# Kernel tuning notes

Measured on AMD Instinct MI355X. Metric: run time of the kernel, lower is better.

Reference implementation:

```python
import jax, jax.numpy as jnp
import numpy as np

NPOINT = 1024
RADIUS = 0.9
NSAMPLE = 32
MLP = [64, 64, 128]
IN_CH = 67
BN_EPS = 1e-5


def setup_inputs() -> dict:
    key = jax.random.key(0)
    ks = jax.random.split(key, 2 + 2 * len(MLP))
    B, N, C = 16, 4096, 64
    inp = {}
    inp["xyz"] = jax.random.uniform(ks[0], (B, N, 3), dtype=jnp.float32)
    inp["points"] = jax.random.normal(ks[1], (B, N, C), dtype=jnp.float32)
    last = IN_CH
    for i, oc in enumerate(MLP):
        inp[f"w{i}"] = jax.random.normal(ks[2 + 2 * i], (oc, last), dtype=jnp.float32) * (1.0 / np.sqrt(last))
        inp[f"b{i}"] = jax.random.normal(ks[3 + 2 * i], (oc,), dtype=jnp.float32) * 0.01
        inp[f"g{i}"] = jnp.ones((oc,), jnp.float32)
        inp[f"beta{i}"] = jnp.zeros((oc,), jnp.float32)
        last = oc
    return inp


def _farthest_point_sample(xyz, npoint):
    # Sequential FPS; initial farthest index fixed to 0 (torch used randint) for determinism.
    B, N, _ = xyz.shape

    def step(carry, _):
        distance, far = carry
        cen = jnp.take_along_axis(xyz, far[:, None, None], axis=1)  # [B,1,3]
        d = jnp.sum((xyz - cen) ** 2, -1)                            # [B,N]
        distance = jnp.minimum(distance, d)
        new_far = jnp.argmax(distance, axis=-1).astype(jnp.int32)
        return (distance, new_far), far

    init = (jnp.full((B, N), 1e10, xyz.dtype), jnp.zeros((B,), jnp.int32))
    _, cents = jax.lax.scan(step, init, None, length=npoint)  # [npoint, B]
    return jnp.transpose(cents)  # [B, npoint]


def _gather(points, idx):
    # points [B,N,C], idx [B,S] or [B,S,K]
    return jax.vmap(lambda p, i: p[i])(points, idx)


def _query_ball_point(radius, nsample, xyz, new_xyz):
    # Faithful to source: Euclidean distance (cdist p=2) compared against radius**2.
    B, N, _ = xyz.shape
    d2 = (jnp.sum(new_xyz ** 2, -1)[:, :, None]
          + jnp.sum(xyz ** 2, -1)[:, None, :]
          - 2.0 * jnp.einsum('bsc,bnc->bsn', new_xyz, xyz))
    dist = jnp.sqrt(jnp.maximum(d2, 0.0))                  # [B,S,N]
    arang = jnp.arange(N, dtype=jnp.int32)[None, None, :]
    gi = jnp.where(dist > radius ** 2, N, arang)           # [B,S,N]
    gi = jnp.sort(gi, axis=-1)[:, :, :nsample]             # [B,S,K]
    first = gi[:, :, :1]
    gi = jnp.where(gi == N, first, gi)
    return gi


def _forward(xyz, points, params):
    idx = _farthest_point_sample(xyz, NPOINT)              # [B,S]
    new_xyz = _gather(xyz, idx)                            # [B,S,3]
    gidx = _query_ball_point(RADIUS, NSAMPLE, xyz, new_xyz)
    grouped_xyz = _gather(xyz, gidx)                       # [B,S,K,3]
    grouped_xyz_norm = grouped_xyz - new_xyz[:, :, None, :]
    grouped_pts = _gather(points, gidx)                    # [B,S,K,C]
    x = jnp.concatenate([grouped_xyz_norm, grouped_pts], axis=-1)  # [B,S,K,3+C]
    x = jnp.transpose(x, (0, 3, 1, 2))                     # [B,Cin,S,K]
    for (w, b, g, be) in params:
        x = jnp.einsum('oc,bcsk->bosk', w, x) + b[None, :, None, None]
        mu = jnp.mean(x, axis=(0, 2, 3), keepdims=True)    # BN in training mode (batch stats, biased var)
        var = jnp.mean((x - mu) ** 2, axis=(0, 2, 3), keepdims=True)
        x = (x - mu) / jnp.sqrt(var + BN_EPS) * g[None, :, None, None] + be[None, :, None, None]
        x = jax.nn.relu(x)
    new_points = jnp.max(x, axis=-1)                       # [B,Cout,S]
    new_points = jnp.transpose(new_points, (0, 2, 1))      # [B,S,Cout]
    return new_xyz, new_points


def reference(xyz, points, w0, b0, g0, beta0, w1, b1, g1, beta1, w2, b2, g2, beta2):
    params = [(w0, b0, g0, beta0), (w1, b1, g1, beta1), (w2, b2, g2, beta2)]
    return _forward(xyz, points, params)
```

## Files before the change

### kernel.cpp

```cpp
#include <hip/hip_runtime.h>
#include <hip/hip_bf16.h>
#include <stdint.h>

#define BB 16
#define NN 4096
#define NPOINT 1024
#define NSAMPLE 32

typedef unsigned int u32;
typedef unsigned long long u64;
typedef unsigned short u16;
typedef float f32x2 __attribute__((ext_vector_type(2)));
using frag_ab = __attribute__((ext_vector_type(8))) short;
using frag_cd = __attribute__((ext_vector_type(4))) float;

__device__ inline u16 f2bf(float x){ u32 u = __float_as_uint(x); u32 r = (u + 0x7fffu + ((u>>16)&1u)) >> 16; return (u16)r; }
__device__ inline float bf2f(u32 hbits){ return __uint_as_float(hbits<<16); }
__device__ inline u64 umax64(u64 a, u64 b){ return a > b ? a : b; }

__device__ inline int wave_max_bits(float v){
    int x = __float_as_int(v);
    int t;
    t = __builtin_amdgcn_update_dpp(0, x, 0x111, 0xf, 0xf, true);
    x = __float_as_int(fmaxf(__int_as_float(x), __int_as_float(t)));
    t = __builtin_amdgcn_update_dpp(0, x, 0x112, 0xf, 0xf, true);
    x = __float_as_int(fmaxf(__int_as_float(x), __int_as_float(t)));
    t = __builtin_amdgcn_update_dpp(0, x, 0x114, 0xf, 0xf, true);
    x = __float_as_int(fmaxf(__int_as_float(x), __int_as_float(t)));
    t = __builtin_amdgcn_update_dpp(0, x, 0x118, 0xf, 0xf, true);
    x = __float_as_int(fmaxf(__int_as_float(x), __int_as_float(t)));
    t = __builtin_amdgcn_update_dpp(0, x, 0x142, 0xf, 0xf, true);
    x = __float_as_int(fmaxf(__int_as_float(x), __int_as_float(t)));
    t = __builtin_amdgcn_update_dpp(0, x, 0x143, 0xf, 0xf, true);
    x = __float_as_int(fmaxf(__int_as_float(x), __int_as_float(t)));
    return __builtin_amdgcn_readlane(x, 63);
}

__global__ __launch_bounds__(256) void fps_kernel(const float* __restrict__ xyz, int* __restrict__ cents)
{
#pragma clang fp contract(off)
    __shared__ float lxyz[NN*3];
    __shared__ __align__(16) u64 s_red[2][4];
    const int tid = threadIdx.x;
    const int b = blockIdx.x;
    const float* gx = xyz + (size_t)b*NN*3;
    for (int i = tid; i < NN*3; i += 256) lxyz[i] = gx[i];
    __syncthreads();
    f32x2 px[8], py[8], pz[8], dist[8];
#pragma unroll
    for (int jj = 0; jj < 8; jj++){
        int p = tid*16 + jj*2;
        px[jj] = (f32x2){ lxyz[p*3+0], lxyz[(p+1)*3+0] };
        py[jj] = (f32x2){ lxyz[p*3+1], lxyz[(p+1)*3+1] };
        pz[jj] = (f32x2){ lxyz[p*3+2], lxyz[(p+1)*3+2] };
        dist[jj] = (f32x2){ 1e10f, 1e10f };
    }
    const int lane = tid & 63;
    const int wid = tid >> 6;
    int far = 0, par = 0;
    for (int s = 0; s < NPOINT; s++){
        if (tid == 0) cents[b*NPOINT + s] = far;
        float cx = lxyz[far*3+0], cy = lxyz[far*3+1], cz = lxyz[far*3+2];
        f32x2 c2x = { cx, cx }, c2y = { cy, cy }, c2z = { cz, cz };
        f32x2 bm0 = { -1.f, -1.f }, bm1 = { -1.f, -1.f };
#pragma unroll
        for (int jj = 0; jj < 8; jj++){
            f32x2 dx = px[jj] - c2x;
            f32x2 dy = py[jj] - c2y;
            f32x2 dz = pz[jj] - c2z;
            f32x2 d  = (dx*dx + dy*dy) + dz*dz;
            f32x2 nd = __builtin_elementwise_min(dist[jj], d);
            dist[jj] = nd;
            if (jj < 4) bm0 = __builtin_elementwise_max(bm0, nd);
            else        bm1 = __builtin_elementwise_max(bm1, nd);
        }
        f32x2 bmA = __builtin_elementwise_max(bm0, bm1);
        float bv = fmaxf(bmA.x, bmA.y);
        int wmb = wave_max_bits(bv);
        float wmax = __int_as_float(wmb);
        u64 mask = __ballot(bv == wmax);
        int fl = __ffsll((long long)mask) - 1;
        float g0m = fmaxf(bm0.x, bm0.y);
        int gsel = (g0m == wmax) ? 0 : 1;
        u32 mbits = 0;
#pragma unroll
        for (int u = 0; u < 4; u++){
            f32x2 dd = gsel ? dist[4+u] : dist[u];
            if (dd.x == wmax) mbits |= (1u << (2*u));
            if (dd.y == wmax) mbits |= (1u << (2*u+1));
        }
        int fj = (gsel << 3) + (__ffs(mbits) - 1);
        int fjw = __builtin_amdgcn_readlane(fj, fl);
        int p = (wid << 10) + (fl << 4) + fjw;
        if (lane == 0) s_red[par][wid] = ((u64)(u32)wmb << 32) | (u32)(4095 - p);
        __syncthreads();
        uint4 k01 = *(const uint4*)&s_red[par][0];
        uint4 k23 = *(const uint4*)&s_red[par][2];
        u64 r0 = ((u64)k01.y << 32) | k01.x;
        u64 r1 = ((u64)k01.w << 32) | k01.z;
        u64 r2 = ((u64)k23.y << 32) | k23.x;
        u64 r3 = ((u64)k23.w << 32) | k23.z;
        u64 m  = umax64(umax64(r0, r1), umax64(r2, r3));
        far = 4095 - (int)(m & 0xFFFu);
        par ^= 1;
    }
}

__global__ __launch_bounds__(256) void gather_newxyz_kernel(const float* __restrict__ xyz, const int* __restrict__ cents,
                                                            float* __restrict__ out, float* __restrict__ nxyz)
{
    int i = blockIdx.x*256 + threadIdx.x;
    int b = i / 3072;
    int r = i - b*3072;
    int s = r / 3;
    int c = r - s*3;
    int idx = cents[b*NPOINT + s];
    float v = xyz[((size_t)b*NN + idx)*3 + c];
    out[i] = v;
    nxyz[i] = v;
}

__global__ __launch_bounds__(256) void pack_points_kernel(const float* __restrict__ points, u32* __restrict__ pbf)
{
    int i = blockIdx.x*256 + threadIdx.x;
    float f0 = points[2*i], f1 = points[2*i+1];
    pbf[i] = (u32)f2bf(f0) | ((u32)f2bf(f1) << 16);
}

__global__ __launch_bounds__(256) void ballquery_kernel(const float* __restrict__ xyz, const float* __restrict__ nxyz,
                                                        const int* __restrict__ cents, int* __restrict__ gidx)
{
    const int lane = threadIdx.x & 63;
    const int w = (blockIdx.x << 2) + (threadIdx.x >> 6);
    const int b = w >> 10;
    const float RAD2 = (float)(0.9*0.9);
    const float* c3 = nxyz + (size_t)w*3;
    float cx = c3[0], cy = c3[1], cz = c3[2];
    float sc = __fadd_rn(__fadd_rn(__fmul_rn(cx,cx), __fmul_rn(cy,cy)), __fmul_rn(cz,cz));
    const float* gx = xyz + (size_t)b*NN*3;
    int* gout = gidx + (size_t)w*NSAMPLE;
    int found = 0; int first = -1;
    for (int base = 0; base < NN; base += 64){
        int i = base + lane;
        float pxv = gx[i*3+0], pyv = gx[i*3+1], pzv = gx[i*3+2];
        float sp = __fadd_rn(__fadd_rn(__fmul_rn(pxv,pxv), __fmul_rn(pyv,pyv)), __fmul_rn(pzv,pzv));
        float dot = __fadd_rn(__fadd_rn(__fmul_rn(cx,pxv), __fmul_rn(cy,pyv)), __fmul_rn(cz,pzv));
        float d2 = __fsub_rn(__fadd_rn(sc, sp), __fmul_rn(2.0f, dot));
        float dd = __fsqrt_rn(fmaxf(d2, 0.0f));
        bool in = !(dd > RAD2);
        u64 m = __ballot(in);
        int cnt = __popcll(m);
        if (in){
            int slot = found + __popcll(m & ((1ull<<lane) - 1ull));
            if (slot < NSAMPLE) gout[slot] = i;
        }
        if (found == 0 && cnt > 0) first = base + (__ffsll(m) - 1);
        found += cnt;
        if (found >= NSAMPLE) break;
    }
    if (found < NSAMPLE){
        if (found == 0) first = cents[w];
        for (int slot = found + lane; slot < NSAMPLE; slot += 64) gout[slot] = first;
    }
}

__global__ __launch_bounds__(256) void conv1_kernel(const float* __restrict__ xyz, const u32* __restrict__ pbf,
                                                    const float* __restrict__ nxyz, const int* __restrict__ gidx,
                                                    const float* __restrict__ w, const float* __restrict__ bias,
                                                    u32* __restrict__ xout, float* __restrict__ stats)
{
    __shared__ float sxyz[512][3];
    const int tid = threadIdx.x;
    const int lane = tid & 63;
    const int wid = tid >> 6;
    const int quad = lane >> 4;
    const int col = lane & 15;
    const int blockbase = blockIdx.x*512;
    for (int r = tid; r < 512; r += 256){
        int m = blockbase + r;
        int b = m >> 15, s = (m >> 5) & 1023, g = gidx[m];
        const float* p3 = xyz + ((size_t)(b<<12) + g)*3;
        const float* c3 = nxyz + ((size_t)b*NPOINT + s)*3;
        sxyz[r][0] = p3[0]-c3[0]; sxyz[r][1] = p3[1]-c3[1]; sxyz[r][2] = p3[2]-c3[2];
    }
    frag_ab Bf[4][2];
#pragma unroll
    for (int nt = 0; nt < 4; nt++)
#pragma unroll
        for (int kh = 0; kh < 2; kh++){
            const float* wr = w + (nt*16 + col)*67 + 3 + kh*32 + quad*8;
#pragma unroll
            for (int j = 0; j < 8; j++) Bf[nt][kh][j] = (short)f2bf(wr[j]);
        }
    float wx[4], wy[4], wz[4], biasl[4];
#pragma unroll
    for (int nt = 0; nt < 4; nt++){
        const float* wb = w + (nt*16 + col)*67;
        wx[nt] = wb[0]; wy[nt] = wb[1]; wz[nt] = wb[2];
        biasl[nt] = bias[nt*16 + col];
    }
    __syncthreads();
    float ssum[4] = {0,0,0,0}, ssq[4] = {0,0,0,0};
    u16* xo = (u16*)xout;
    const int tile0 = blockIdx.x*32 + wid*8;
#pragma unroll 2
    for (int t = 0; t < 8; t++){
        const int tile = tile0 + t;
        const size_t m0 = (size_t)tile * 16;
        const int b = (int)(m0 >> 15);
        const int g = gidx[m0 + col];
        const u32* arow = pbf + ((size_t)(b<<12) + g)*32;
        uint4 u0 = *(const uint4*)(arow + quad*4);
        uint4 u1 = *(const uint4*)(arow + 16 + quad*4);
        frag_ab Af0, Af1;
        __builtin_memcpy(&Af0, &u0, 16);
        __builtin_memcpy(&Af1, &u1, 16);
        frag_cd acc[4];
#pragma unroll
        for (int nt = 0; nt < 4; nt++){
            acc[nt] = (frag_cd){0.f, 0.f, 0.f, 0.f};
            acc[nt] = __builtin_amdgcn_mfma_f32_16x16x32_bf16(Af0, Bf[nt][0], acc[nt], 0, 0, 0);
            acc[nt] = __builtin_amdgcn_mfma_f32_16x16x32_bf16(Af1, Bf[nt][1], acc[nt], 0, 0, 0);
        }
        const int rbase = (int)(m0 - blockbase) + quad*4;
#pragma unroll
        for (int r = 0; r < 4; r++){
            float xnx = sxyz[rbase+r][0], xny = sxyz[rbase+r][1], xnz = sxyz[rbase+r][2];
#pragma unroll
            for (int nt = 0; nt < 4; nt++){
                float v = acc[nt][r] + biasl[nt];
                v = fmaf(wx[nt], xnx, v);
                v = fmaf(wy[nt], xny, v);
                v = fmaf(wz[nt], xnz, v);
                xo[(m0 + quad*4 + r)*64 + nt*16 + col] = f2bf(v);
                ssum[nt] += v;
                ssq[nt] = fmaf(v, v, ssq[nt]);
            }
        }
    }
#pragma unroll
    for (int nt = 0; nt < 4; nt++){
        ssum[nt] += __shfl_xor(ssum[nt], 16); ssq[nt] += __shfl_xor(ssq[nt], 16);
        ssum[nt] += __shfl_xor(ssum[nt], 32); ssq[nt] += __shfl_xor(ssq[nt], 32);
    }
    if (quad == 0){
        float* st = stats + (blockIdx.x & 7)*256;
#pragma unroll
        for (int nt = 0; nt < 4; nt++){
            atomicAdd(&st[nt*16 + col], ssum[nt]);
            atomicAdd(&st[128 + nt*16 + col], ssq[nt]);
        }
    }
}

__device__ inline void block_finalize(const float* __restrict__ stats, const float* __restrict__ g,
                                      const float* __restrict__ beta, float* saff, int C, int tid)
{
    if (tid < C){
        float sm = 0.f, sq = 0.f;
#pragma unroll
        for (int r = 0; r < 8; r++){ sm += stats[r*256+tid]; sq += stats[r*256+128+tid]; }
        const float invM = 1.0f / 524288.0f;
        float mu  = sm * invM;
        float var = fmaxf(sq * invM - mu*mu, 0.0f);
        float inv = 1.0f / sqrtf(var + 1e-5f);
        float a = g[tid] * inv;
        saff[tid] = a;
        saff[128+tid] = beta[tid] - mu*a;
    }
}

__device__ inline void unpack_affine_relu(uint4 u, const float* ak, const float* bk, short* dst){
    const u32* uu = (const u32*)&u;
#pragma unroll
    for (int q = 0; q < 4; q++){
        u32 v = uu[q];
        float x0 = bf2f(v & 0xffffu);
        float x1 = bf2f(v >> 16);
        float f0 = fmaxf(fmaf(ak[2*q],   x0, bk[2*q]),   0.f);
        float f1 = fmaxf(fmaf(ak[2*q+1], x1, bk[2*q+1]), 0.f);
        dst[2*q]   = (short)f2bf(f0);
        dst[2*q+1] = (short)f2bf(f1);
    }
}

__global__ __launch_bounds__(256) void conv2_kernel(const u32* __restrict__ xin, const float* __restrict__ stats_in,
                                                    const float* __restrict__ gw, const float* __restrict__ beta,
                                                    const float* __restrict__ w, const float* __restrict__ bias,
                                                    u32* __restrict__ xout, float* __restrict__ stats)
{
    __shared__ float saff[256];
    const int tid = threadIdx.x;
    block_finalize(stats_in, gw, beta, saff, 64, tid);
    const int lane = tid & 63;
    const int wid = tid >> 6;
    const int quad = lane >> 4;
    const int col = lane & 15;
    frag_ab Bf[4][2];
#pragma unroll
    for (int nt = 0; nt < 4; nt++)
#pragma unroll
        for (int kh = 0; kh < 2; kh++){
            const float* wr = w + (nt*16 + col)*64 + kh*32 + quad*8;
#pragma unroll
            for (int j = 0; j < 8; j++) Bf[nt][kh][j] = (short)f2bf(wr[j]);
        }
    float biasl[4];
#pragma unroll
    for (int nt = 0; nt < 4; nt++) biasl[nt] = bias[nt*16 + col];
    __syncthreads();
    float ak[2][8], bk[2][8];
#pragma unroll
    for (int kh = 0; kh < 2; kh++)
#pragma unroll
        for (int j = 0; j < 8; j++){
            int k = kh*32 + quad*8 + j;
            ak[kh][j] = saff[k]; bk[kh][j] = saff[128+k];
        }
    float ssum[4] = {0,0,0,0}, ssq[4] = {0,0,0,0};
    u16* xo = (u16*)xout;
    const int tile0 = blockIdx.x*64 + wid*16;
    for (int t = 0; t < 16; t++){
        const size_t m0 = (size_t)(tile0 + t) * 16;
        const u32* arow = xin + (m0 + col)*32;
        uint4 u0 = *(const uint4*)(arow + quad*4);
        uint4 u1 = *(const uint4*)(arow + 16 + quad*4);
        frag_ab Af0, Af1;
        unpack_affine_relu(u0, ak[0], bk[0], (short*)&Af0);
        unpack_affine_relu(u1, ak[1], bk[1], (short*)&Af1);
        frag_cd acc[4];
#pragma unroll
        for (int nt = 0; nt < 4; nt++){
            acc[nt] = (frag_cd){biasl[nt], biasl[nt], biasl[nt], biasl[nt]};
            acc[nt] = __builtin_amdgcn_mfma_f32_16x16x32_bf16(Af0, Bf[nt][0], acc[nt], 0, 0, 0);
            acc[nt] = __builtin_amdgcn_mfma_f32_16x16x32_bf16(Af1, Bf[nt][1], acc[nt], 0, 0, 0);
        }
#pragma unroll
        for (int nt = 0; nt < 4; nt++){
#pragma unroll
            for (int r = 0; r < 4; r++){
                float v = acc[nt][r];
                xo[(m0 + quad*4 + r)*64 + nt*16 + col] = f2bf(v);
                ssum[nt] += v;
                ssq[nt] = fmaf(v, v, ssq[nt]);
            }
        }
    }
#pragma unroll
    for (int nt = 0; nt < 4; nt++){
        ssum[nt] += __shfl_xor(ssum[nt], 16); ssq[nt] += __shfl_xor(ssq[nt], 16);
        ssum[nt] += __shfl_xor(ssum[nt], 32); ssq[nt] += __shfl_xor(ssq[nt], 32);
    }
    if (quad == 0){
        float* st = stats + (blockIdx.x & 7)*256;
#pragma unroll
        for (int nt = 0; nt < 4; nt++){
            atomicAdd(&st[nt*16 + col], ssum[nt]);
            atomicAdd(&st[128 + nt*16 + col], ssq[nt]);
        }
    }
}

__global__ __launch_bounds__(256) void conv3_kernel(const u32* __restrict__ xin, const float* __restrict__ stats_in,
                                                    const float* __restrict__ gw, const float* __restrict__ beta,
                                                    const float* __restrict__ w, const float* __restrict__ bias,
                                                    float* __restrict__ gmax, float* __restrict__ gmin,
                                                    float* __restrict__ stats)
{
    __shared__ float saff[256];
    const int tid = threadIdx.x;
    block_finalize(stats_in, gw, beta, saff, 64, tid);
    const int lane = tid & 63;
    const int wid = tid >> 6;
    const int quad = lane >> 4;
    const int col = lane & 15;
    frag_ab Bf[8][2];
#pragma unroll
    for (int nt = 0; nt < 8; nt++)
#pragma unroll
        for (int kh = 0; kh < 2; kh++){
            const float* wr = w + (nt*16 + col)*64 + kh*32 + quad*8;
#pragma unroll
            for (int j = 0; j < 8; j++) Bf[nt][kh][j] = (short)f2bf(wr[j]);
        }
    float biasl[8];
#pragma unroll
    for (int nt = 0; nt < 8; nt++) biasl[nt] = bias[nt*16 + col];
    __syncthreads();
    float ak[2][8], bk[2][8];
#pragma unroll
    for (int kh = 0; kh < 2; kh++)
#pragma unroll
        for (int j = 0; j < 8; j++){
            int k = kh*32 + quad*8 + j;
            ak[kh][j] = saff[k]; bk[kh][j] = saff[128+k];
        }
    float ssum[8], ssq[8], mx[8], mn[8];
#pragma unroll
    for (int nt = 0; nt < 8; nt++){ ssum[nt] = 0.f; ssq[nt] = 0.f; }
    const int tile0 = blockIdx.x*32 + wid*8;
#pragma unroll 2
    for (int t = 0; t < 8; t++){
        const size_t m0 = (size_t)(tile0 + t) * 16;
        const u32* arow = xin + (m0 + col)*32;
        uint4 u0 = *(const uint4*)(arow + quad*4);
        uint4 u1 = *(const uint4*)(arow + 16 + quad*4);
        frag_ab Af0, Af1;
        unpack_affine_relu(u0, ak[0], bk[0], (short*)&Af0);
        unpack_affine_relu(u1, ak[1], bk[1], (short*)&Af1);
        frag_cd acc[8];
#pragma unroll
        for (int nt = 0; nt < 8; nt++){
            acc[nt] = (frag_cd){biasl[nt], biasl[nt], biasl[nt], biasl[nt]};
            acc[nt] = __builtin_amdgcn_mfma_f32_16x16x32_bf16(Af0, Bf[nt][0], acc[nt], 0, 0, 0);
            acc[nt] = __builtin_amdgcn_mfma_f32_16x16x32_bf16(Af1, Bf[nt][1], acc[nt], 0, 0, 0);
        }
#pragma unroll
        for (int nt = 0; nt < 8; nt++){
            float a0 = fmaxf(fmaxf(acc[nt][0], acc[nt][1]), fmaxf(acc[nt][2], acc[nt][3]));
            float n0 = fminf(fminf(acc[nt][0], acc[nt][1]), fminf(acc[nt][2], acc[nt][3]));
            if ((t & 1) == 0){ mx[nt] = a0; mn[nt] = n0; }
            else { mx[nt] = fmaxf(mx[nt], a0); mn[nt] = fminf(mn[nt], n0); }
#pragma unroll
            for (int r = 0; r < 4; r++){
                float v = acc[nt][r];
                ssum[nt] += v;
                ssq[nt] = fmaf(v, v, ssq[nt]);
            }
        }
        if (t & 1){
#pragma unroll
            for (int nt = 0; nt < 8; nt++){
                mx[nt] = fmaxf(mx[nt], __shfl_xor(mx[nt], 16));
                mn[nt] = fminf(mn[nt], __shfl_xor(mn[nt], 16));
                mx[nt] = fmaxf(mx[nt], __shfl_xor(mx[nt], 32));
                mn[nt] = fminf(mn[nt], __shfl_xor(mn[nt], 32));
            }
            if (quad == 0){
                const int g = (tile0 + t - 1) >> 1;
#pragma unroll
                for (int nt = 0; nt < 8; nt++){
                    gmax[(size_t)g*128 + nt*16 + col] = mx[nt];
                    gmin[(size_t)g*128 + nt*16 + col] = mn[nt];
                }
            }
        }
    }
#pragma unroll
    for (int nt = 0; nt < 8; nt++){
        ssum[nt] += __shfl_xor(ssum[nt], 16); ssq[nt] += __shfl_xor(ssq[nt], 16);
        ssum[nt] += __shfl_xor(ssum[nt], 32); ssq[nt] += __shfl_xor(ssq[nt], 32);
    }
    if (quad == 0){
        float* st = stats + (blockIdx.x & 7)*256;
#pragma unroll
        for (int nt = 0; nt < 8; nt++){
            atomicAdd(&st[nt*16 + col], ssum[nt]);
            atomicAdd(&st[128 + nt*16 + col], ssq[nt]);
        }
    }
}

__global__ __launch_bounds__(256) void pool_kernel(const float* __restrict__ gmax, const float* __restrict__ gmin,
                                                   const float* __restrict__ stats_in, const float* __restrict__ gw,
                                                   const float* __restrict__ beta, float* __restrict__ out)
{
    __shared__ float saff[256];
    const int tid = threadIdx.x;
    block_finalize(stats_in, gw, beta, saff, 128, tid);
    __syncthreads();
    const int base = blockIdx.x*2048 + tid;
#pragma unroll
    for (int k = 0; k < 8; k++){
        int idx = base + k*256;
        int o = idx & 127;
        float a = saff[o], bsh = saff[128+o];
        float v = (a >= 0.f) ? fmaf(a, gmax[idx], bsh) : fmaf(a, gmin[idx], bsh);
        out[(size_t)BB*NPOINT*3 + idx] = fmaxf(v, 0.f);
    }
}

extern "C" void kernel_launch(void* const* d_in, const int* in_sizes, int n_in,
                              void* d_out, int out_size, void* d_ws, size_t ws_size,
                              hipStream_t stream)
{
    const float* xyz    = (const float*)d_in[0];
    const float* points = (const float*)d_in[1];
    const float* w0  = (const float*)d_in[2];
    const float* b0  = (const float*)d_in[3];
    const float* g0  = (const float*)d_in[4];
    const float* be0 = (const float*)d_in[5];
    const float* w1  = (const float*)d_in[6];
    const float* b1  = (const float*)d_in[7];
    const float* g1  = (const float*)d_in[8];
    const float* be1 = (const float*)d_in[9];
    const float* w2  = (const float*)d_in[10];
    const float* b2  = (const float*)d_in[11];
    const float* g2  = (const float*)d_in[12];
    const float* be2 = (const float*)d_in[13];
    float* out = (float*)d_out;
    char* ws = (char*)d_ws;

    int*   cents = (int*)(ws + 0);
    float* nxyz  = (float*)(ws + 65536);
    int*   gidx  = (int*)(ws + 262144);
    float* stats = (float*)(ws + 2359296);
    u32*   x1buf = (u32*)(ws + 2386944);
    u32*   x2buf = (u32*)(ws + 69495808);
    float* gmax  = (float*)(ws + 136604672);
    float* gmin  = (float*)(ws + 144993280);
    u32*   pbf   = (u32*)(ws + 136604672);

    hipMemsetAsync(stats, 0, 6144*sizeof(float), stream);
    fps_kernel<<<16, 256, 0, stream>>>(xyz, cents);
    gather_newxyz_kernel<<<192, 256, 0, stream>>>(xyz, cents, out, nxyz);
    pack_points_kernel<<<8192, 256, 0, stream>>>(points, pbf);
    ballquery_kernel<<<4096, 256, 0, stream>>>(xyz, nxyz, cents, gidx);
    conv1_kernel<<<1024, 256, 0, stream>>>(xyz, pbf, nxyz, gidx, w0, b0, x1buf, stats);
    conv2_kernel<<<512, 256, 0, stream>>>(x1buf, stats, g0, be0, w1, b1, x2buf, stats + 2048);
    conv3_kernel<<<1024, 256, 0, stream>>>(x2buf, stats + 2048, g1, be1, w2, b2, gmax, gmin, stats + 4096);
    pool_kernel<<<1024, 256, 0, stream>>>(gmax, gmin, stats + 4096, g2, be2, out);
}
```

Before: 803.5 us.

## Replace FPS block barrier with tagged LDS spin-wait and forward centroid coordinates

In the farthest-point-sampling loop, the per-iteration __syncthreads is replaced by a flag-based spin-wait. Each wave publishes its max distance, its index and a step tag to LDS, and all threads poll until all four waves have written the current tag. Each wave also publishes the coordinates of its candidate point, so the next centroid comes straight from the reduction instead of a dependent LDS load of lxyz[far]. The per-thread argmax is now tracked inline during the distance update, replacing the separate rescan for matching lanes. The risks are relying on volatile LDS ordering without explicit fences, and a 12-bit tag that wraps, though 1024 steps with double buffering stays within range.

```diff
diff --git a/kernel.cpp b/kernel.cpp
--- a/kernel.cpp
+++ b/kernel.cpp
@@ -16,7 +16,6 @@
 
 __device__ inline u16 f2bf(float x){ u32 u = __float_as_uint(x); u32 r = (u + 0x7fffu + ((u>>16)&1u)) >> 16; return (u16)r; }
 __device__ inline float bf2f(u32 hbits){ return __uint_as_float(hbits<<16); }
-__device__ inline u64 umax64(u64 a, u64 b){ return a > b ? a : b; }
 
 __device__ inline int wave_max_bits(float v){
     int x = __float_as_int(v);
@@ -40,11 +39,13 @@
 {
 #pragma clang fp contract(off)
     __shared__ float lxyz[NN*3];
-    __shared__ __align__(16) u64 s_red[2][4];
+    __shared__ __align__(16) u32 sK[2][8];
+    __shared__ __align__(16) float sC[2][4][4];
     const int tid = threadIdx.x;
     const int b = blockIdx.x;
     const float* gx = xyz + (size_t)b*NN*3;
     for (int i = tid; i < NN*3; i += 256) lxyz[i] = gx[i];
+    if (tid < 8){ sK[0][tid] = 0; sK[1][tid] = 0; }
     __syncthreads();
     f32x2 px[8], py[8], pz[8], dist[8];
 #pragma unroll
@@ -58,50 +59,64 @@
     const int lane = tid & 63;
     const int wid = tid >> 6;
     int far = 0, par = 0;
+    float cx = lxyz[0], cy = lxyz[1], cz = lxyz[2];
     for (int s = 0; s < NPOINT; s++){
         if (tid == 0) cents[b*NPOINT + s] = far;
-        float cx = lxyz[far*3+0], cy = lxyz[far*3+1], cz = lxyz[far*3+2];
         f32x2 c2x = { cx, cx }, c2y = { cy, cy }, c2z = { cz, cz };
-        f32x2 bm0 = { -1.f, -1.f }, bm1 = { -1.f, -1.f };
+        float bv = -1.0f; int bj = 0;
 #pragma unroll
         for (int jj = 0; jj < 8; jj++){
             f32x2 dx = px[jj] - c2x;
             f32x2 dy = py[jj] - c2y;
             f32x2 dz = pz[jj] - c2z;
             f32x2 d  = (dx*dx + dy*dy) + dz*dz;
-            f32x2 nd = __builtin_elementwise_min(dist[jj], d);
+            f32x2 nd;
+            nd.x = fminf(dist[jj].x, d.x);
+            nd.y = fminf(dist[jj].y, d.y);
             dist[jj] = nd;
-            if (jj < 4) bm0 = __builtin_elementwise_max(bm0, nd);
-            else        bm1 = __builtin_elementwise_max(bm1, nd);
-        }
-        f32x2 bmA = __builtin_elementwise_max(bm0, bm1);
-        float bv = fmaxf(bmA.x, bmA.y);
+            if (nd.x > bv){ bv = nd.x; bj = jj*2; }
+            if (nd.y > bv){ bv = nd.y; bj = jj*2+1; }
+        }
+        const int p_loc = tid*16 + bj;
+        float sx = lxyz[p_loc*3+0], sy = lxyz[p_loc*3+1], sz = lxyz[p_loc*3+2];
         int wmb = wave_max_bits(bv);
         float wmax = __int_as_float(wmb);
         u64 mask = __ballot(bv == wmax);
         int fl = __ffsll((long long)mask) - 1;
-        float g0m = fmaxf(bm0.x, bm0.y);
-        int gsel = (g0m == wmax) ? 0 : 1;
-        u32 mbits = 0;
-#pragma unroll
-        for (int u = 0; u < 4; u++){
-            f32x2 dd = gsel ? dist[4+u] : dist[u];
-            if (dd.x == wmax) mbits |= (1u << (2*u));
-            if (dd.y == wmax) mbits |= (1u << (2*u+1));
-        }
-        int fj = (gsel << 3) + (__ffs(mbits) - 1);
-        int fjw = __builtin_amdgcn_readlane(fj, fl);
-        int p = (wid << 10) + (fl << 4) + fjw;
-        if (lane == 0) s_red[par][wid] = ((u64)(u32)wmb << 32) | (u32)(4095 - p);
-        __syncthreads();
-        uint4 k01 = *(const uint4*)&s_red[par][0];
-        uint4 k23 = *(const uint4*)&s_red[par][2];
-        u64 r0 = ((u64)k01.y << 32) | k01.x;
-        u64 r1 = ((u64)k01.w << 32) | k01.z;
-        u64 r2 = ((u64)k23.y << 32) | k23.x;
-        u64 r3 = ((u64)k23.w << 32) | k23.z;
-        u64 m  = umax64(umax64(r0, r1), umax64(r2, r3));
-        far = 4095 - (int)(m & 0xFFFu);
+        int pw = __builtin_amdgcn_readlane(p_loc, fl);
+        float qx = __int_as_float(__builtin_amdgcn_readlane(__float_as_int(sx), fl));
+        float qy = __int_as_float(__builtin_amdgcn_readlane(__float_as_int(sy), fl));
+        float qz = __int_as_float(__builtin_amdgcn_readlane(__float_as_int(sz), fl));
+        const u32 tag = (u32)(s + 1);
+        if (lane == 0){
+            volatile float* vc = &sC[par][wid][0];
+            vc[0] = qx; vc[1] = qy; vc[2] = qz;
+            volatile u32* vk = &sK[par][wid*2];
+            vk[0] = (u32)wmb;
+            vk[1] = ((u32)(4095 - pw) << 12) | tag;
+        }
+        volatile u32* vk = &sK[par][0];
+        u32 t0, t1, t2, t3;
+        for (;;){
+            t0 = vk[1]; t1 = vk[3]; t2 = vk[5]; t3 = vk[7];
+            if ((((t0 ^ tag) | (t1 ^ tag) | (t2 ^ tag) | (t3 ^ tag)) & 0xFFFu) == 0) break;
+        }
+        u32 d0 = vk[0], d1 = vk[2], d2 = vk[4], d3 = vk[6];
+        volatile float* vc = &sC[par][0][0];
+        float x0 = vc[0],  y0 = vc[1],  z0 = vc[2];
+        float x1 = vc[4],  y1 = vc[5],  z1 = vc[6];
+        float x2v= vc[8],  y2 = vc[9],  z2 = vc[10];
+        float x3 = vc[12], y3 = vc[13], z3 = vc[14];
+        u64 k0 = ((u64)d0 << 32) | t0;
+        u64 k1 = ((u64)d1 << 32) | t1;
+        u64 k2 = ((u64)d2 << 32) | t2;
+        u64 k3 = ((u64)d3 << 32) | t3;
+        u64 bk = k0; float bx = x0, by = y0, bz = z0;
+        if (k1 > bk){ bk = k1; bx = x1;  by = y1; bz = z1; }
+        if (k2 > bk){ bk = k2; bx = x2v; by = y2; bz = z2; }
+        if (k3 > bk){ bk = k3; bx = x3;  by = y3; bz = z3; }
+        far = 4095 - (int)(((u32)bk >> 12) & 0xFFFu);
+        cx = bx; cy = by; cz = bz;
         par ^= 1;
     }
 }
```

Result: slower. 1.474 ms (+83.4%).
